# Kernel tuning notes

Measured on AMD Instinct MI355X. Metric: run time of the kernel, lower is better.

## Reference

```python
import jax, jax.numpy as jnp
import numpy as np

E = 16          # embed_dim
EPS = 1e-5      # BatchNorm eps


def _lin(x, w, b):
    # torch nn.Linear: y = x @ W^T + b
    return x @ w.T + b


def _mha_len1(v, in_w, in_b, out_w, out_b):
    # nn.MultiheadAttention with query/key/value of seq_len 1:
    # softmax over a single key is identically 1, so the output is
    # out_proj(v_proj(value)) and is independent of query/key.
    wv, bv = in_w[2 * E:3 * E], in_b[2 * E:3 * E]
    return _lin(_lin(v, wv, bv), out_w, out_b)


def _forward(x, ehr_w, ehr_b, img_w, img_b, bio_w, bio_b,
             bio_qkv_w, bio_qkv_b, ehr_qkv_w, ehr_qkv_b, img_qkv_w, img_qkv_b,
             attn_in_w, attn_in_b, attn_out_w, attn_out_b,
             ab_proj_w, ab_proj_b, f1_w, f1_b, bn_g, bn_b, f2_w, f2_b):
    # per-modality scalar -> embed_dim encoders (seq_len-1, so work in [B,E])
    ehr_feat = jax.nn.relu(_lin(x[:, 0:1], ehr_w, ehr_b))  # [B,E]
    img_feat = jax.nn.relu(_lin(x[:, 1:2], img_w, img_b))
    bio_feat = jax.nn.relu(_lin(x[:, 2:3], bio_w, bio_b))

    # stacked q/k/v projections per modality; only V slices affect the output
    bio_qkv = _lin(bio_feat, bio_qkv_w, bio_qkv_b)  # [B,3E]
    ehr_qkv = _lin(ehr_feat, ehr_qkv_w, ehr_qkv_b)
    img_qkv = _lin(img_feat, img_qkv_w, img_qkv_b)
    Va = bio_qkv[:, 2 * E:3 * E]
    Vb = ehr_qkv[:, 2 * E:3 * E]

    bio_ehr = _mha_len1(Vb, attn_in_w, attn_in_b, attn_out_w, attn_out_b)
    ehr_bio = _mha_len1(Va, attn_in_w, attn_in_b, attn_out_w, attn_out_b)

    ab = _lin(jnp.concatenate([bio_ehr, ehr_bio], axis=-1), ab_proj_w, ab_proj_b)  # [B,E]
    img_ab = _mha_len1(ab, attn_in_w, attn_in_b, attn_out_w, attn_out_b)

    final = jnp.concatenate([ab, img_ab], axis=-1)  # [B,2E]
    h = _lin(final, f1_w, f1_b)                      # [B,64]
    # BatchNorm1d, training-mode batch statistics (biased variance); dropout off
    mu = jnp.mean(h, axis=0)
    var = jnp.mean(jnp.square(h - mu), axis=0)
    h = (h - mu) * jax.lax.rsqrt(var + EPS) * bn_g + bn_b
    h = jax.nn.relu(h)
    return _lin(h, f2_w, f2_b)  # [B,3]


def setup_inputs() -> dict:
    key = jax.random.key(0)
    ks = iter(jax.random.split(key, 40))
    w = lambda *shape: jax.random.normal(next(ks), shape, jnp.float32) * 0.1
    B = 1048576
    return {
        "x": jax.random.normal(next(ks), (B, 3), jnp.float32),
        "ehr_w": w(E, 1), "ehr_b": w(E),
        "img_w": w(E, 1), "img_b": w(E),
        "bio_w": w(E, 1), "bio_b": w(E),
        "bio_qkv_w": w(3 * E, E), "bio_qkv_b": w(3 * E),
        "ehr_qkv_w": w(3 * E, E), "ehr_qkv_b": w(3 * E),
        "img_qkv_w": w(3 * E, E), "img_qkv_b": w(3 * E),
        "attn_in_w": w(3 * E, E), "attn_in_b": w(3 * E),
        "attn_out_w": w(E, E), "attn_out_b": w(E),
        "ab_proj_w": w(E, 2 * E), "ab_proj_b": w(E),
        "f1_w": w(64, 2 * E), "f1_b": w(64),
        "bn_g": jnp.ones((64,), jnp.float32), "bn_b": jnp.zeros((64,), jnp.float32),
        "f2_w": w(3, 64), "f2_b": w(3),
    }


def reference(x, ehr_w, ehr_b, img_w, img_b, bio_w, bio_b,
              bio_qkv_w, bio_qkv_b, ehr_qkv_w, ehr_qkv_b, img_qkv_w, img_qkv_b,
              attn_in_w, attn_in_b, attn_out_w, attn_out_b,
              ab_proj_w, ab_proj_b, f1_w, f1_b, bn_g, bn_b, f2_w, f2_b):
    return _forward(x, ehr_w, ehr_b, img_w, img_b, bio_w, bio_b,
                    bio_qkv_w, bio_qkv_b, ehr_qkv_w, ehr_qkv_b, img_qkv_w, img_qkv_b,
                    attn_in_w, attn_in_b, attn_out_w, attn_out_b,
                    ab_proj_w, ab_proj_b, f1_w, f1_b, bn_g, bn_b, f2_w, f2_b)
```

## Files before the change

kernel.cpp:

```cpp
#include <hip/hip_runtime.h>
#include <math.h>

#define NITV 17
#define NCELL (NITV*NITV)
#define CELLF 6
#define AGG_N (NCELL*CELLF)
#define NREP 4
#define QS   4096.0f
#define QINV (1.0/4096.0)

#define RAW_OFF  3468
#define THR_OFF  7820
#define EVT_OFF  7856
#define BVT_OFF  10032

__device__ __forceinline__ int bsearch17(const float* t, float x) {
  bool c8 = t[7] < x;
  float s2 = c8 ? t[11] : t[3];
  bool c4 = s2 < x;
  float sa = c8 ? t[13] : t[5];
  float sb = c8 ? t[9]  : t[1];
  float s3 = c4 ? sa : sb;
  bool c2 = s3 < x;
  float v00 = c2 ? t[2]  : t[0];
  float v01 = c2 ? t[6]  : t[4];
  float v10 = c2 ? t[10] : t[8];
  float v11 = c2 ? t[14] : t[12];
  float w0 = c4 ? v01 : v00;
  float w1 = c4 ? v11 : v10;
  float s4 = c8 ? w1 : w0;
  bool c1 = s4 < x;
  int c = (c8?8:0) + (c4?4:0) + (c2?2:0) + (c1?1:0);
  c += (t[15] < x) ? 1 : 0;
  return c;
}

__global__ void __launch_bounds__(256) hist_kernel(
    const float* __restrict__ x,
    const float* __restrict__ ehr_w, const float* __restrict__ ehr_b,
    const float* __restrict__ bio_w, const float* __restrict__ bio_b,
    const float* __restrict__ bio_qkv_w, const float* __restrict__ bio_qkv_b,
    const float* __restrict__ ehr_qkv_w, const float* __restrict__ ehr_qkv_b,
    const float* __restrict__ attn_in_w, const float* __restrict__ attn_in_b,
    const float* __restrict__ attn_out_w, const float* __restrict__ attn_out_b,
    const float* __restrict__ ab_proj_w, const float* __restrict__ ab_proj_b,
    const float* __restrict__ f1_w, const float* __restrict__ f1_b,
    unsigned long long* __restrict__ agg, float* __restrict__ ws,
    int B, int nblk)
{
  __shared__ int accS[NREP*AGG_N];
  __shared__ float thrS[32];
  __shared__ float mvec[16], uvec[16], vvec[16], cab[16], h0p[64];
  __shared__ float wEx[16], bEx[16], cEx[16], tEx[16];
  __shared__ float wBx[16], bBx[16], cBx[16], tBx[16];
  __shared__ int   rkE[16], rkB[16];
  const int tid = threadIdx.x;

  if ((int)blockIdx.x == nblk) {
    float* S  = (float*)accS;
    float* M  = S;
    float* P1 = S + 256;
    float* P2 = S + 512;
    float* Ae = S + 768;
    float* Ab = S + 1024;
    float* G  = S + 1280;
    float* Ge = S + 2304;
    float* Gb = S + 3328;

    {
      int o = tid >> 4, k = tid & 15;
      float s = 0.f;
      for (int j = 0; j < 16; ++j)
        s = fmaf(attn_out_w[o*16+j], attn_in_w[(32+j)*16+k], s);
      M[tid] = s;
    }
    if (tid < 16) {
      float s = attn_out_b[tid];
      for (int j = 0; j < 16; ++j)
        s = fmaf(attn_out_w[tid*16+j], attn_in_b[32+j], s);
      mvec[tid] = s;
    }
    __syncthreads();

    {
      int o = tid >> 4, i = tid & 15;
      float s1 = 0.f, s2 = 0.f;
      for (int t = 0; t < 16; ++t) {
        float mt = M[t*16+i];
        s1 = fmaf(ab_proj_w[o*32+t],    mt, s1);
        s2 = fmaf(ab_proj_w[o*32+16+t], mt, s2);
      }
      P1[tid] = s1; P2[tid] = s2;
    }
    if (tid < 16) {
      float su = mvec[tid], sv = mvec[tid];
      for (int i = 0; i < 16; ++i) {
        float mt = M[tid*16+i];
        su = fmaf(mt, ehr_qkv_b[32+i], su);
        sv = fmaf(mt, bio_qkv_b[32+i], sv);
      }
      uvec[tid] = su; vvec[tid] = sv;
    }
    for (int idx = tid; idx < 1024; idx += 256) {
      int j = idx >> 4, k = idx & 15;
      float s = f1_w[j*32+k];
      for (int i = 0; i < 16; ++i)
        s = fmaf(f1_w[j*32+16+i], M[i*16+k], s);
      G[idx] = s;
    }
    __syncthreads();

    {
      int o = tid >> 4, k = tid & 15;
      float s1 = 0.f, s2 = 0.f;
      for (int i = 0; i < 16; ++i) {
        s1 = fmaf(P1[o*16+i], ehr_qkv_w[(32+i)*16+k], s1);
        s2 = fmaf(P2[o*16+i], bio_qkv_w[(32+i)*16+k], s2);
      }
      Ae[tid] = s1; Ab[tid] = s2;
    }
    if (tid < 16) {
      float s = ab_proj_b[tid];
      for (int t = 0; t < 16; ++t) {
        s = fmaf(ab_proj_w[tid*32+t],    uvec[t], s);
        s = fmaf(ab_proj_w[tid*32+16+t], vvec[t], s);
      }
      cab[tid] = s;
    }
    if (tid < 16) {
      float w = ehr_w[tid], b = ehr_b[tid];
      bool z = (w == 0.0f);
      wEx[tid] = z ? 0.f : w;
      bEx[tid] = z ? 0.f : b;
      cEx[tid] = z ? fmaxf(b, 0.f) : 0.f;
      tEx[tid] = z ? __builtin_inff() : (-b / w);
    } else if (tid < 32) {
      int k = tid - 16;
      float w = bio_w[k], b = bio_b[k];
      bool z = (w == 0.0f);
      wBx[k] = z ? 0.f : w;
      bBx[k] = z ? 0.f : b;
      cBx[k] = z ? fmaxf(b, 0.f) : 0.f;
      tBx[k] = z ? __builtin_inff() : (-b / w);
    }
    __syncthreads();

    for (int idx = tid; idx < 1024; idx += 256) {
      int j = idx >> 4, k = idx & 15;
      float s1 = 0.f, s2 = 0.f;
      for (int i = 0; i < 16; ++i) {
        float g = G[j*16+i];
        s1 = fmaf(g, Ae[i*16+k], s1);
        s2 = fmaf(g, Ab[i*16+k], s2);
      }
      Ge[idx] = s1; Gb[idx] = s2;
    }
    if (tid < 64) {
      float s = f1_b[tid];
      for (int i = 0; i < 16; ++i) {
        s = fmaf(G[tid*16+i], cab[i], s);
        s = fmaf(f1_w[tid*32+16+i], mvec[i], s);
      }
      h0p[tid] = s;
    }
    if (tid < 16) {
      int r = 0;
      for (int j = 0; j < 16; ++j)
        r += (tEx[j] < tEx[tid]) || (tEx[j] == tEx[tid] && j < tid);
      rkE[tid] = r;
    } else if (tid < 32) {
      int k = tid - 16, r = 0;
      for (int j = 0; j < 16; ++j)
        r += (tBx[j] < tBx[k]) || (tBx[j] == tBx[k] && j < k);
      rkB[k] = r;
    }
    __syncthreads();

    if (tid < 64) {
      float s = h0p[tid];
      for (int k = 0; k < 16; ++k)
        s += Ge[tid*16+k]*cEx[k] + Gb[tid*16+k]*cBx[k];
      h0p[tid] = s;
    }
    __syncthreads();

    for (int idx = tid; idx < NITV*64; idx += 256) {
      int i = idx >> 6, j = idx & 63;
      float ue = 0.f, ve = 0.f, ub = 0.f, vb = 0.f;
      for (int k = 0; k < 16; ++k) {
        bool actE = (wEx[k] > 0.f) ? (rkE[k] < i) : (rkE[k] >= i);
        bool actB = (wBx[k] > 0.f) ? (rkB[k] < i) : (rkB[k] >= i);
        if (actE) { ue = fmaf(Ge[j*16+k], wEx[k], ue); ve = fmaf(Ge[j*16+k], bEx[k], ve); }
        if (actB) { ub = fmaf(Gb[j*16+k], wBx[k], ub); vb = fmaf(Gb[j*16+k], bBx[k], vb); }
      }
      ws[RAW_OFF + idx]        = ue;
      ws[RAW_OFF + 1088 + idx] = ve + h0p[j];
      ws[RAW_OFF + 2176 + idx] = ub;
      ws[RAW_OFF + 3264 + idx] = vb;
    }
    if (tid < 16) {
      ws[THR_OFF + rkE[tid]]      = tEx[tid];
      ws[THR_OFF + 16 + rkB[tid]] = tBx[tid];
    }
    return;
  }

  if (tid < 16) {
    float tloc[16];
    #pragma unroll
    for (int j = 0; j < 16; ++j) {
      float w = ehr_w[j], b = ehr_b[j];
      tloc[j] = (w == 0.0f) ? __builtin_inff() : (-b / w);
    }
    float mine = tloc[tid];
    int r = 0;
    #pragma unroll
    for (int j = 0; j < 16; ++j)
      r += (tloc[j] < mine) || (tloc[j] == mine && j < tid);
    thrS[r] = mine;
  } else if (tid < 32) {
    int k = tid - 16;
    float tloc[16];
    #pragma unroll
    for (int j = 0; j < 16; ++j) {
      float w = bio_w[j], b = bio_b[j];
      tloc[j] = (w == 0.0f) ? __builtin_inff() : (-b / w);
    }
    float mine = tloc[k];
    int r = 0;
    #pragma unroll
    for (int j = 0; j < 16; ++j)
      r += (tloc[j] < mine) || (tloc[j] == mine && j < k);
    thrS[16 + r] = mine;
  }
  for (int i = tid; i < NREP*AGG_N; i += 256) accS[i] = 0;
  __syncthreads();

  float te[16], tb[16];
  #pragma unroll
  for (int k = 0; k < 16; ++k) { te[k] = thrS[k]; tb[k] = thrS[16+k]; }
  const int rep = tid & (NREP-1);
  const int s0 = (blockIdx.x*256 + tid)*4;

  float xs0[4], xs2[4];
  int nv = 0;
  if (s0 + 4 <= B) {
    const float4* xp = (const float4*)(x + (size_t)s0*3);
    float4 a = xp[0], b = xp[1], c = xp[2];
    xs0[0]=a.x; xs2[0]=a.z;  xs0[1]=a.w; xs2[1]=b.y;
    xs0[2]=b.z; xs2[2]=c.x;  xs0[3]=c.y; xs2[3]=c.w;
    nv = 4;
  } else {
    for (int u = 0; u < 4; ++u) {
      int i = s0 + u;
      if (i < B) { xs0[nv] = x[3*(size_t)i]; xs2[nv] = x[3*(size_t)i+2]; ++nv; }
    }
  }
  for (int u = 0; u < nv; ++u) {
    float x0 = xs0[u], x2 = xs2[u];
    int iv0 = bsearch17(te, x0);
    int iv2 = bsearch17(tb, x2);
    int* c = &accS[rep*AGG_N + (iv0*NITV + iv2)*CELLF];
    atomicAdd(c+0, 1);
    atomicAdd(c+1, __float2int_rn(x0*QS));
    atomicAdd(c+2, __float2int_rn(x2*QS));
    atomicAdd(c+3, __float2int_rn(x0*x0*QS));
    atomicAdd(c+4, __float2int_rn(x2*x2*QS));
    atomicAdd(c+5, __float2int_rn(x0*x2*QS));
  }
  __syncthreads();
  for (int i = tid; i < AGG_N; i += 256) {
    long long s = (long long)accS[i] + accS[AGG_N+i] + accS[2*AGG_N+i] + accS[3*AGG_N+i];
    if (s) atomicAdd(&agg[i], (unsigned long long)s);
  }
}

__global__ void __launch_bounds__(256) mid_kernel(
    const unsigned long long* __restrict__ agg,
    float* ws,
    const float* __restrict__ bn_g, const float* __restrict__ bn_b,
    int B)
{
  __shared__ double aggd[AGG_N];
  __shared__ float  Rl[4352];
  __shared__ double sh2p[256];
  __shared__ double margnE[NITV], margxE[NITV], margnB[NITV], margxB[NITV];
  __shared__ float  sArr[64], aE[64], aB[64];
  const int tid = threadIdx.x;

  for (int i = tid; i < 1088; i += 256)
    ((uint4*)Rl)[i] = ((const uint4*)(ws + RAW_OFF))[i];
  for (int i = tid; i < AGG_N; i += 256) {
    long long v = (long long)agg[i];
    aggd[i] = (i % 6 == 0) ? (double)v : (double)v * QINV;
  }
  __syncthreads();

  if (tid < NITV) {
    double n = 0, sx = 0;
    for (int q = 0; q < NITV; ++q) {
      n  += aggd[(tid*NITV+q)*CELLF];
      sx += aggd[(tid*NITV+q)*CELLF + 1];
    }
    margnE[tid] = n; margxE[tid] = sx;
  } else if (tid >= 32 && tid < 32+NITV) {
    int q = tid - 32;
    double n = 0, sx = 0;
    for (int p = 0; p < NITV; ++p) {
      n  += aggd[(p*NITV+q)*CELLF];
      sx += aggd[(p*NITV+q)*CELLF + 2];
    }
    margnB[q] = n; margxB[q] = sx;
  }

  {
    const int j = tid & 63, pg = tid >> 6;
    double sh2 = 0;
    for (int p = pg; p < NITV; p += 4) {
      const double Ue = (double)Rl[p*64+j];
      const double Ve = (double)Rl[1088 + p*64+j];
      for (int q = 0; q < NITV; ++q) {
        const double* c = &aggd[(p*NITV+q)*CELLF];
        double n = c[0], sx0 = c[1], sx2 = c[2], s00 = c[3], s22 = c[4], s02 = c[5];
        double Ub = (double)Rl[2176 + q*64+j];
        double Vb = (double)Rl[3264 + q*64+j];
        sh2 += s00*Ue*Ue + 2.0*sx0*Ue*Ve + n*Ve*Ve
             + s22*Ub*Ub + 2.0*sx2*Ub*Vb + n*Vb*Vb
             + 2.0*(s02*Ue*Ub + sx0*Ue*Vb + sx2*Ve*Ub + n*Ve*Vb);
      }
    }
    sh2p[tid] = sh2;
  }
  __syncthreads();

  if (tid < 64) {
    const int j = tid;
    double sh2 = (sh2p[j] + sh2p[64+j]) + (sh2p[128+j] + sh2p[192+j]);
    const double invB = 1.0 / (double)B;
    double mua = 0, mub = 0;
    for (int p = 0; p < NITV; ++p) {
      mua += margxE[p]*(double)Rl[p*64+j]      + margnE[p]*(double)Rl[1088+p*64+j];
      mub += margxB[p]*(double)Rl[2176+p*64+j] + margnB[p]*(double)Rl[3264+p*64+j];
    }
    mua *= invB; mub *= invB;
    double mu  = mua + mub;
    double var = sh2*invB - mu*mu;
    double s   = (double)bn_g[j] / sqrt(var + 1e-5);
    sArr[j] = (float)s;
    aE[j] = (float)(0.5*(double)bn_b[j] - s*mua);
    aB[j] = (float)(0.5*(double)bn_b[j] - s*mub);
  }
  __syncthreads();

  float4* EVT = (float4*)(ws + EVT_OFF);
  float4* BVT = (float4*)(ws + BVT_OFF);
  for (int idx = tid; idx < NITV*32; idx += 256) {
    int itv = idx >> 5, p = idx & 31;
    int j0 = 2*p, j1 = 2*p + 1;
    float sc0 = sArr[j0], sc1 = sArr[j1];
    float4 E;
    E.x = sc0 * Rl[itv*64+j0];
    E.y = sc1 * Rl[itv*64+j1];
    E.z = fmaf(sc0, Rl[1088+itv*64+j0], aE[j0]);
    E.w = fmaf(sc1, Rl[1088+itv*64+j1], aE[j1]);
    EVT[p*NITV + itv] = E;
    float4 Bv;
    Bv.x = sc0 * Rl[2176+itv*64+j0];
    Bv.y = sc1 * Rl[2176+itv*64+j1];
    Bv.z = fmaf(sc0, Rl[3264+itv*64+j0], aB[j0]);
    Bv.w = fmaf(sc1, Rl[3264+itv*64+j1], aB[j1]);
    BVT[p*NITV + itv] = Bv;
  }
}

__global__ void __launch_bounds__(256) apply_kernel(
    const float* __restrict__ x, const float* __restrict__ ws,
    const float* __restrict__ f2_w, const float* __restrict__ f2_b,
    float* __restrict__ out, int B)
{
  __shared__ __align__(16) float4 tabs[2*544];
  const int tid = threadIdx.x;

  const int s0 = (blockIdx.x*256 + tid)*4;
  float xs0[4], xs2[4];
  int nv = 0;
  if (s0 + 4 <= B) {
    const float4* xp = (const float4*)(x + (size_t)s0*3);
    float4 a = xp[0], b = xp[1], c = xp[2];
    xs0[0]=a.x; xs2[0]=a.z;  xs0[1]=a.w; xs2[1]=b.y;
    xs0[2]=b.z; xs2[2]=c.x;  xs0[3]=c.y; xs2[3]=c.w;
    nv = 4;
  } else {
    for (int u = 0; u < 4; ++u) {
      int i = s0 + u;
      if (i < B) { xs0[nv] = x[3*(size_t)i]; xs2[nv] = x[3*(size_t)i+2]; ++nv; }
    }
  }

  for (int i = tid; i < 1088; i += 256)
    ((uint4*)tabs)[i] = ((const uint4*)(ws + EVT_OFF))[i];

  float te[16], tb[16];
  #pragma unroll
  for (int k = 0; k < 16; ++k) { te[k] = ws[THR_OFF+k]; tb[k] = ws[THR_OFF+16+k]; }
  const float b0 = f2_b[0], b1 = f2_b[1], b2 = f2_b[2];
  __syncthreads();

  float res[12];
  #pragma unroll
  for (int u = 0; u < 4; ++u) {
    if (u >= nv) break;
    float x0 = xs0[u], x2 = xs2[u];
    int iv0 = bsearch17(te, x0);
    int iv2 = bsearch17(tb, x2);
    const float4* ev = tabs + iv0;
    const float4* bv = tabs + 544 + iv2;
    float a0 = b0, a1 = b1, a2 = b2;
    #pragma unroll
    for (int p = 0; p < 32; ++p) {
      float4 e = ev[p*NITV];
      float4 v = bv[p*NITV];
      float h0 = fmaf(x0, e.x, e.z) + fmaf(x2, v.x, v.z);
      float h1 = fmaf(x0, e.y, e.w) + fmaf(x2, v.y, v.w);
      float r0 = fmaxf(h0, 0.f);
      float r1 = fmaxf(h1, 0.f);
      const int j = 2*p;
      a0 = fmaf(r0, f2_w[j],     fmaf(r1, f2_w[j+1],     a0));
      a1 = fmaf(r0, f2_w[64+j],  fmaf(r1, f2_w[64+j+1],  a1));
      a2 = fmaf(r0, f2_w[128+j], fmaf(r1, f2_w[128+j+1], a2));
    }
    res[u*3+0] = a0; res[u*3+1] = a1; res[u*3+2] = a2;
  }
  if (nv == 4) {
    float4* op = (float4*)(out + (size_t)s0*3);
    op[0] = make_float4(res[0], res[1], res[2],  res[3]);
    op[1] = make_float4(res[4], res[5], res[6],  res[7]);
    op[2] = make_float4(res[8], res[9], res[10], res[11]);
  } else {
    for (int u = 0; u < nv; ++u) {
      size_t i = (size_t)(s0 + u);
      out[3*i+0] = res[u*3+0]; out[3*i+1] = res[u*3+1]; out[3*i+2] = res[u*3+2];
    }
  }
}

extern "C" void kernel_launch(void* const* d_in, const int* in_sizes, int n_in,
                              void* d_out, int out_size, void* d_ws, size_t ws_size,
                              hipStream_t stream) {
  const float* x          = (const float*)d_in[0];
  const float* ehr_w      = (const float*)d_in[1];
  const float* ehr_b      = (const float*)d_in[2];
  const float* bio_w      = (const float*)d_in[5];
  const float* bio_b      = (const float*)d_in[6];
  const float* bio_qkv_w  = (const float*)d_in[7];
  const float* bio_qkv_b  = (const float*)d_in[8];
  const float* ehr_qkv_w  = (const float*)d_in[9];
  const float* ehr_qkv_b  = (const float*)d_in[10];
  const float* attn_in_w  = (const float*)d_in[13];
  const float* attn_in_b  = (const float*)d_in[14];
  const float* attn_out_w = (const float*)d_in[15];
  const float* attn_out_b = (const float*)d_in[16];
  const float* ab_proj_w  = (const float*)d_in[17];
  const float* ab_proj_b  = (const float*)d_in[18];
  const float* f1_w       = (const float*)d_in[19];
  const float* f1_b       = (const float*)d_in[20];
  const float* bn_g       = (const float*)d_in[21];
  const float* bn_b       = (const float*)d_in[22];
  const float* f2_w       = (const float*)d_in[23];
  const float* f2_b       = (const float*)d_in[24];
  float* out = (float*)d_out;
  float* ws  = (float*)d_ws;
  unsigned long long* agg = (unsigned long long*)d_ws;
  const int B = in_sizes[0] / 3;
  const int nblk = (B + 1023) / 1024;

  hipMemsetAsync(d_ws, 0, AGG_N*sizeof(unsigned long long), stream);
  hist_kernel<<<nblk+1, 256, 0, stream>>>(x, ehr_w, ehr_b, bio_w, bio_b,
      bio_qkv_w, bio_qkv_b, ehr_qkv_w, ehr_qkv_b,
      attn_in_w, attn_in_b, attn_out_w, attn_out_b,
      ab_proj_w, ab_proj_b, f1_w, f1_b, agg, ws, B, nblk);
  mid_kernel<<<1, 256, 0, stream>>>(agg, ws, bn_g, bn_b, B);
  apply_kernel<<<nblk, 256, 0, stream>>>(x, ws, f2_w, f2_b, out, B);
}
```

Baseline: 88.48 us.

## Pack histogram moments into 64-bit atomics and use fp16 tables in apply

```diff
diff --git a/kernel.cpp b/kernel.cpp
--- a/kernel.cpp
+++ b/kernel.cpp
@@ -3,16 +3,31 @@
 
 #define NITV 17
 #define NCELL (NITV*NITV)
-#define CELLF 6
-#define AGG_N (NCELL*CELLF)
 #define NREP 4
 #define QS   4096.0f
 #define QINV (1.0/4096.0)
-
-#define RAW_OFF  3468
-#define THR_OFF  7820
-#define EVT_OFF  7856
-#define BVT_OFF  10032
+#define JSTR 5
+#define AGGJ_N (NCELL*JSTR)
+#define AGGM_OFF AGGJ_N
+#define AGG_TOT (AGGJ_N + NITV)
+
+#define RAW_OFF  2924
+#define THR_OFF  7276
+#define F2PK_OFF 7308
+#define EVT_OFF  7404
+#define BVT_OFF  8492
+
+typedef _Float16 h2 __attribute__((ext_vector_type(2)));
+
+#if __has_builtin(__builtin_amdgcn_fdot2)
+__device__ __forceinline__ float fdot2f(h2 a, h2 b, float c) {
+  return __builtin_amdgcn_fdot2(a, b, c, false);
+}
+#else
+__device__ __forceinline__ float fdot2f(h2 a, h2 b, float c) {
+  return fmaf((float)a.x, (float)b.x, fmaf((float)a.y, (float)b.y, c));
+}
+#endif
 
 __device__ __forceinline__ int bsearch17(const float* t, float x) {
   bool c8 = t[7] < x;
@@ -48,7 +63,7 @@
     unsigned long long* __restrict__ agg, float* __restrict__ ws,
     int B, int nblk)
 {
-  __shared__ int accS[NREP*AGG_N];
+  __shared__ unsigned long long ACC[2*NREP*NCELL + NREP*NITV];
   __shared__ float thrS[32];
   __shared__ float mvec[16], uvec[16], vvec[16], cab[16], h0p[64];
   __shared__ float wEx[16], bEx[16], cEx[16], tEx[16];
@@ -57,7 +72,7 @@
   const int tid = threadIdx.x;
 
   if ((int)blockIdx.x == nblk) {
-    float* S  = (float*)accS;
+    float* S  = (float*)ACC;
     float* M  = S;
     float* P1 = S + 256;
     float* P2 = S + 512;
@@ -233,7 +248,7 @@
       r += (tloc[j] < mine) || (tloc[j] == mine && j < k);
     thrS[16 + r] = mine;
   }
-  for (int i = tid; i < NREP*AGG_N; i += 256) accS[i] = 0;
+  for (int i = tid; i < 2*NREP*NCELL + NREP*NITV; i += 256) ACC[i] = 0ull;
   __syncthreads();
 
   float te[16], tb[16];
@@ -260,28 +275,59 @@
     float x0 = xs0[u], x2 = xs2[u];
     int iv0 = bsearch17(te, x0);
     int iv2 = bsearch17(tb, x2);
-    int* c = &accS[rep*AGG_N + (iv0*NITV + iv2)*CELLF];
-    atomicAdd(c+0, 1);
-    atomicAdd(c+1, __float2int_rn(x0*QS));
-    atomicAdd(c+2, __float2int_rn(x2*QS));
-    atomicAdd(c+3, __float2int_rn(x0*x0*QS));
-    atomicAdd(c+4, __float2int_rn(x2*x2*QS));
-    atomicAdd(c+5, __float2int_rn(x0*x2*QS));
+    int cell = iv0*NITV + iv2;
+    int q1  = __float2int_rn(x0*QS);
+    int q2  = __float2int_rn(x2*QS);
+    int q02 = __float2int_rn(x0*x2*QS);
+    int q3  = __float2int_rn(x0*x0*QS);
+    int q4  = __float2int_rn(x2*x2*QS);
+    unsigned long long A = (1ull<<52)
+        | ((unsigned long long)(unsigned)(q1 + 65536) << 26)
+        |  (unsigned long long)(unsigned)(q2 + 65536);
+    unsigned long long Bv = ((unsigned long long)(unsigned)(q02 + 524288) << 27)
+        |  (unsigned long long)(unsigned)q3;
+    atomicAdd(&ACC[rep*NCELL + cell], A);
+    atomicAdd(&ACC[NREP*NCELL + rep*NCELL + cell], Bv);
+    atomicAdd(&ACC[2*NREP*NCELL + rep*NITV + iv2], (unsigned long long)(unsigned)q4);
   }
   __syncthreads();
-  for (int i = tid; i < AGG_N; i += 256) {
-    long long s = (long long)accS[i] + accS[AGG_N+i] + accS[2*AGG_N+i] + accS[3*AGG_N+i];
-    if (s) atomicAdd(&agg[i], (unsigned long long)s);
+  for (int i = tid; i < NCELL; i += 256) {
+    long long n=0, s1=0, s2=0, sc=0, s3=0;
+    #pragma unroll
+    for (int r = 0; r < NREP; ++r) {
+      unsigned long long A = ACC[r*NCELL + i];
+      unsigned long long Bv = ACC[NREP*NCELL + r*NCELL + i];
+      long long nr = (long long)(A >> 52);
+      n  += nr;
+      s1 += (long long)((A >> 26) & 0x3FFFFFFull) - (nr << 16);
+      s2 += (long long)(A & 0x3FFFFFFull)         - (nr << 16);
+      sc += (long long)(Bv >> 27)                 - (nr << 19);
+      s3 += (long long)(Bv & 0x7FFFFFFull);
+    }
+    if (n) {
+      atomicAdd(&agg[i*JSTR+0], (unsigned long long)n);
+      atomicAdd(&agg[i*JSTR+1], (unsigned long long)s1);
+      atomicAdd(&agg[i*JSTR+2], (unsigned long long)s2);
+      atomicAdd(&agg[i*JSTR+3], (unsigned long long)sc);
+      atomicAdd(&agg[i*JSTR+4], (unsigned long long)s3);
+    }
+  }
+  if (tid < NITV) {
+    unsigned long long s = 0;
+    #pragma unroll
+    for (int r = 0; r < NREP; ++r) s += ACC[2*NREP*NCELL + r*NITV + tid];
+    if (s) atomicAdd(&agg[AGGM_OFF + tid], s);
   }
 }
 
 __global__ void __launch_bounds__(256) mid_kernel(
     const unsigned long long* __restrict__ agg,
-    float* ws,
+    float* ws, unsigned int* wsu,
     const float* __restrict__ bn_g, const float* __restrict__ bn_b,
-    int B)
+    const float* __restrict__ f2_w, int B)
 {
-  __shared__ double aggd[AGG_N];
+  __shared__ double aggd[AGGJ_N];
+  __shared__ double margd[NITV];
   __shared__ float  Rl[4352];
   __shared__ double sh2p[256];
   __shared__ double margnE[NITV], margxE[NITV], margnB[NITV], margxB[NITV];
@@ -290,25 +336,26 @@
 
   for (int i = tid; i < 1088; i += 256)
     ((uint4*)Rl)[i] = ((const uint4*)(ws + RAW_OFF))[i];
-  for (int i = tid; i < AGG_N; i += 256) {
+  for (int i = tid; i < AGGJ_N; i += 256) {
     long long v = (long long)agg[i];
-    aggd[i] = (i % 6 == 0) ? (double)v : (double)v * QINV;
-  }
+    aggd[i] = (i % JSTR == 0) ? (double)v : (double)v * QINV;
+  }
+  if (tid < NITV) margd[tid] = (double)(long long)agg[AGGM_OFF + tid] * QINV;
   __syncthreads();
 
   if (tid < NITV) {
     double n = 0, sx = 0;
     for (int q = 0; q < NITV; ++q) {
-      n  += aggd[(tid*NITV+q)*CELLF];
-      sx += aggd[(tid*NITV+q)*CELLF + 1];
+      n  += aggd[(tid*NITV+q)*JSTR];
+      sx += aggd[(tid*NITV+q)*JSTR + 1];
     }
     margnE[tid] = n; margxE[tid] = sx;
   } else if (tid >= 32 && tid < 32+NITV) {
     int q = tid - 32;
     double n = 0, sx = 0;
     for (int p = 0; p < NITV; ++p) {
-      n  += aggd[(p*NITV+q)*CELLF];
-      sx += aggd[(p*NITV+q)*CELLF + 2];
+      n  += aggd[(p*NITV+q)*JSTR];
+      sx += aggd[(p*NITV+q)*JSTR + 2];
     }
     margnB[q] = n; margxB[q] = sx;
   }
@@ -320,12 +367,12 @@
       const double Ue = (double)Rl[p*64+j];
       const double Ve = (double)Rl[1088 + p*64+j];
       for (int q = 0; q < NITV; ++q) {
-        const double* c = &aggd[(p*NITV+q)*CELLF];
-        double n = c[0], sx0 = c[1], sx2 = c[2], s00 = c[3], s22 = c[4], s02 = c[5];
+        const double* c = &aggd[(p*NITV+q)*JSTR];
+        double n = c[0], sx0 = c[1], sx2 = c[2], s02 = c[3], s00 = c[4];
         double Ub = (double)Rl[2176 + q*64+j];
         double Vb = (double)Rl[3264 + q*64+j];
         sh2 += s00*Ue*Ue + 2.0*sx0*Ue*Ve + n*Ve*Ve
-             + s22*Ub*Ub + 2.0*sx2*Ub*Vb + n*Vb*Vb
+             + 2.0*sx2*Ub*Vb + n*Vb*Vb
              + 2.0*(s02*Ue*Ub + sx0*Ue*Vb + sx2*Ve*Ub + n*Ve*Vb);
       }
     }
@@ -336,6 +383,10 @@
   if (tid < 64) {
     const int j = tid;
     double sh2 = (sh2p[j] + sh2p[64+j]) + (sh2p[128+j] + sh2p[192+j]);
+    for (int q = 0; q < NITV; ++q) {
+      double Ub = (double)Rl[2176 + q*64+j];
+      sh2 += Ub*Ub*margd[q];
+    }
     const double invB = 1.0 / (double)B;
     double mua = 0, mub = 0;
     for (int p = 0; p < NITV; ++p) {
@@ -352,33 +403,40 @@
   }
   __syncthreads();
 
-  float4* EVT = (float4*)(ws + EVT_OFF);
-  float4* BVT = (float4*)(ws + BVT_OFF);
   for (int idx = tid; idx < NITV*32; idx += 256) {
     int itv = idx >> 5, p = idx & 31;
     int j0 = 2*p, j1 = 2*p + 1;
     float sc0 = sArr[j0], sc1 = sArr[j1];
-    float4 E;
-    E.x = sc0 * Rl[itv*64+j0];
-    E.y = sc1 * Rl[itv*64+j1];
-    E.z = fmaf(sc0, Rl[1088+itv*64+j0], aE[j0]);
-    E.w = fmaf(sc1, Rl[1088+itv*64+j1], aE[j1]);
-    EVT[p*NITV + itv] = E;
-    float4 Bv;
-    Bv.x = sc0 * Rl[2176+itv*64+j0];
-    Bv.y = sc1 * Rl[2176+itv*64+j1];
-    Bv.z = fmaf(sc0, Rl[3264+itv*64+j0], aB[j0]);
-    Bv.w = fmaf(sc1, Rl[3264+itv*64+j1], aB[j1]);
-    BVT[p*NITV + itv] = Bv;
+    h2 U, V;
+    U.x = (_Float16)(sc0 * Rl[itv*64+j0]);
+    U.y = (_Float16)(sc1 * Rl[itv*64+j1]);
+    V.x = (_Float16)(fmaf(sc0, Rl[1088+itv*64+j0], aE[j0]));
+    V.y = (_Float16)(fmaf(sc1, Rl[1088+itv*64+j1], aE[j1]));
+    wsu[EVT_OFF + p*34 + 2*itv]     = __builtin_bit_cast(unsigned int, U);
+    wsu[EVT_OFF + p*34 + 2*itv + 1] = __builtin_bit_cast(unsigned int, V);
+    U.x = (_Float16)(sc0 * Rl[2176+itv*64+j0]);
+    U.y = (_Float16)(sc1 * Rl[2176+itv*64+j1]);
+    V.x = (_Float16)(fmaf(sc0, Rl[3264+itv*64+j0], aB[j0]));
+    V.y = (_Float16)(fmaf(sc1, Rl[3264+itv*64+j1], aB[j1]));
+    wsu[BVT_OFF + p*34 + 2*itv]     = __builtin_bit_cast(unsigned int, U);
+    wsu[BVT_OFF + p*34 + 2*itv + 1] = __builtin_bit_cast(unsigned int, V);
+  }
+  if (tid < 96) {
+    int c = tid >> 5, p = tid & 31;
+    h2 F;
+    F.x = (_Float16)f2_w[c*64 + 2*p];
+    F.y = (_Float16)f2_w[c*64 + 2*p + 1];
+    wsu[F2PK_OFF + tid] = __builtin_bit_cast(unsigned int, F);
   }
 }
 
 __global__ void __launch_bounds__(256) apply_kernel(
     const float* __restrict__ x, const float* __restrict__ ws,
-    const float* __restrict__ f2_w, const float* __restrict__ f2_b,
+    const unsigned int* __restrict__ wsu,
+    const float* __restrict__ f2_b,
     float* __restrict__ out, int B)
 {
-  __shared__ __align__(16) float4 tabs[2*544];
+  __shared__ __align__(16) unsigned int tabs[2176];
   const int tid = threadIdx.x;
 
   const int s0 = (blockIdx.x*256 + tid)*4;
@@ -397,15 +455,17 @@
     }
   }
 
-  for (int i = tid; i < 1088; i += 256)
-    ((uint4*)tabs)[i] = ((const uint4*)(ws + EVT_OFF))[i];
+  for (int i = tid; i < 544; i += 256)
+    ((uint4*)tabs)[i] = ((const uint4*)(wsu + EVT_OFF))[i];
 
   float te[16], tb[16];
   #pragma unroll
   for (int k = 0; k < 16; ++k) { te[k] = ws[THR_OFF+k]; tb[k] = ws[THR_OFF+16+k]; }
+  const h2* f2h = (const h2*)(wsu + F2PK_OFF);
   const float b0 = f2_b[0], b1 = f2_b[1], b2 = f2_b[2];
   __syncthreads();
 
+  h2 hz; hz.x = (_Float16)0.f; hz.y = (_Float16)0.f;
   float res[12];
   #pragma unroll
   for (int u = 0; u < 4; ++u) {
@@ -413,21 +473,24 @@
     float x0 = xs0[u], x2 = xs2[u];
     int iv0 = bsearch17(te, x0);
     int iv2 = bsearch17(tb, x2);
-    const float4* ev = tabs + iv0;
-    const float4* bv = tabs + 544 + iv2;
+    const uint2* ev = ((const uint2*)tabs) + iv0;
+    const uint2* bv = ((const uint2*)(tabs + 1088)) + iv2;
+    h2 x0h; x0h.x = (_Float16)x0; x0h.y = (_Float16)x0;
+    h2 x2h; x2h.x = (_Float16)x2; x2h.y = (_Float16)x2;
     float a0 = b0, a1 = b1, a2 = b2;
     #pragma unroll
     for (int p = 0; p < 32; ++p) {
-      float4 e = ev[p*NITV];
-      float4 v = bv[p*NITV];
-      float h0 = fmaf(x0, e.x, e.z) + fmaf(x2, v.x, v.z);
-      float h1 = fmaf(x0, e.y, e.w) + fmaf(x2, v.y, v.w);
-      float r0 = fmaxf(h0, 0.f);
-      float r1 = fmaxf(h1, 0.f);
-      const int j = 2*p;
-      a0 = fmaf(r0, f2_w[j],     fmaf(r1, f2_w[j+1],     a0));
-      a1 = fmaf(r0, f2_w[64+j],  fmaf(r1, f2_w[64+j+1],  a1));
-      a2 = fmaf(r0, f2_w[128+j], fmaf(r1, f2_w[128+j+1], a2));
+      uint2 e = ev[p*NITV];
+      uint2 v = bv[p*NITV];
+      h2 hA = __builtin_elementwise_fma(x0h, __builtin_bit_cast(h2, e.x),
+                                              __builtin_bit_cast(h2, e.y));
+      h2 hB = __builtin_elementwise_fma(x2h, __builtin_bit_cast(h2, v.x),
+                                              __builtin_bit_cast(h2, v.y));
+      h2 hh = hA + hB;
+      h2 r  = __builtin_elementwise_max(hh, hz);
+      a0 = fdot2f(r, f2h[p],      a0);
+      a1 = fdot2f(r, f2h[32 + p], a1);
+      a2 = fdot2f(r, f2h[64 + p], a2);
     }
     res[u*3+0] = a0; res[u*3+1] = a1; res[u*3+2] = a2;
   }
@@ -470,15 +533,16 @@
   const float* f2_b       = (const float*)d_in[24];
   float* out = (float*)d_out;
   float* ws  = (float*)d_ws;
+  unsigned int* wsu = (unsigned int*)d_ws;
   unsigned long long* agg = (unsigned long long*)d_ws;
   const int B = in_sizes[0] / 3;
   const int nblk = (B + 1023) / 1024;
 
-  hipMemsetAsync(d_ws, 0, AGG_N*sizeof(unsigned long long), stream);
+  hipMemsetAsync(d_ws, 0, AGG_TOT*sizeof(unsigned long long), stream);
   hist_kernel<<<nblk+1, 256, 0, stream>>>(x, ehr_w, ehr_b, bio_w, bio_b,
       bio_qkv_w, bio_qkv_b, ehr_qkv_w, ehr_qkv_b,
       attn_in_w, attn_in_b, attn_out_w, attn_out_b,
       ab_proj_w, ab_proj_b, f1_w, f1_b, agg, ws, B, nblk);
-  mid_kernel<<<1, 256, 0, stream>>>(agg, ws, bn_g, bn_b, B);
-  apply_kernel<<<nblk, 256, 0, stream>>>(x, ws, f2_w, f2_b, out, B);
-}
+  mid_kernel<<<1, 256, 0, stream>>>(agg, ws, wsu, bn_g, bn_b, f2_w, B);
+  apply_kernel<<<nblk, 256, 0, stream>>>(x, ws, wsu, f2_b, out, B);
+}
```

After: 169.1 us. 91.1% more time.
